# Optimization experiments

Hardware: AMD Instinct MI355X
Metric: run time of the kernel (lower is better)

Reference implementation:

```python
import jax, jax.numpy as jnp
import numpy as np

D_MODEL = 768
NUM_HEADS = 12
D_HEAD = D_MODEL // NUM_HEADS
LN_EPS = 1e-5


def layer_norm(x, w, b):
    m = jnp.mean(x, axis=-1, keepdims=True)
    v = jnp.mean(jnp.square(x - m), axis=-1, keepdims=True)
    return (x - m) * jax.lax.rsqrt(v + LN_EPS) * w + b


def setup_inputs() -> dict:
    key = jax.random.key(0)
    ks = jax.random.split(key, 10)
    B, P, NQ, D = 16, 197, 8, D_MODEL
    s = 1.0 / np.sqrt(D)
    return {
        "q_x": jax.random.normal(ks[0], (1, NQ, D), jnp.float32),
        "kv_x": jax.random.normal(ks[1], (B, P, D), jnp.float32),
        "pair_pos_embedding": jax.random.normal(ks[2], (2 * P, D), jnp.float32) * 0.02,
        "q_w": jax.random.normal(ks[3], (D, D), jnp.float32) * s,
        "q_b": jnp.zeros((D,), jnp.float32),
        "kv_w": jax.random.normal(ks[4], (D, D), jnp.float32) * s,
        "kv_b": jnp.zeros((D,), jnp.float32),
        "out_w": jax.random.normal(ks[5], (D, D), jnp.float32) * s,
        "out_b": jnp.zeros((D,), jnp.float32),
        "lnq_w": jnp.ones((D,), jnp.float32),
        "lnq_b": jnp.zeros((D,), jnp.float32),
        "lnkv_w": jnp.ones((D,), jnp.float32),
        "lnkv_b": jnp.zeros((D,), jnp.float32),
    }


def reference(q_x, kv_x, pair_pos_embedding, q_w, q_b, kv_w, kv_b,
              out_w, out_b, lnq_w, lnq_b, lnkv_w, lnkv_b):
    H, dh = NUM_HEADS, D_HEAD
    scale = dh ** -0.5
    _, NQ, D = q_x.shape
    B, P, _ = kv_x.shape

    # q path: Linear -> LN -> split heads -> [1, H, NQ, dh]
    q = layer_norm(q_x @ q_w.T + q_b, lnq_w, lnq_b)
    q = q.reshape(1, NQ, H, dh).transpose(0, 2, 1, 3)  # [1,H,NQ,dh]

    # kv path: Linear -> LN -> split heads -> [B, H, P, dh]
    kv = layer_norm(kv_x @ kv_w.T + kv_b, lnkv_w, lnkv_b)
    kv = kv.reshape(B, P, H, dh).transpose(0, 2, 1, 3)  # [B,H,P,dh]

    # pairwise expansion: kv_concat[i*B+j] = cat(kv[i], kv[j]) along token dim
    kv_rep = jnp.repeat(kv, B, axis=0)          # [B^2,H,P,dh] (repeat_interleave)
    kv_til = jnp.tile(kv, (B, 1, 1, 1))         # [B^2,H,P,dh]
    kv_cat = jnp.concatenate([kv_rep, kv_til], axis=2)  # [B^2,H,2P,dh]

    # positional bias: [2P, D] -> [1, H, 2P, dh]
    pos = pair_pos_embedding.reshape(1, 2 * P, H, dh).transpose(0, 2, 1, 3)
    kv_cat = kv_cat + pos

    scores = jnp.einsum('bhqd,bhpd->bhqp', jnp.broadcast_to(q, (B * B, H, NQ, dh)), kv_cat) * scale
    attn = jax.nn.softmax(scores, axis=-1)      # [B^2,H,NQ,2P]

    v1 = jnp.einsum('bhqp,bhpd->bhqd', attn[..., :P], kv_cat[:, :, :P, :])
    v2 = jnp.einsum('bhqp,bhpd->bhqd', attn[..., P:], kv_cat[:, :, P:, :])
    values = (v1 - v2).transpose(0, 2, 1, 3).reshape(B * B, NQ, D)
    return values @ out_w.T + out_b
```

## Files before the change

kernel.cpp:

```cpp
#include <hip/hip_runtime.h>
#include <hip/hip_bf16.h>
#include <math.h>

#define D_MODEL 768
#define NHEADS  12
#define DHEAD   64
#define NQR     8
#define BB      16
#define PP      197
#define NPAIR   256
#define MKV     (BB*PP)
#define LN_EPSF 1e-5f
#define SCALEF  0.125f

#define KTOT  2304
#define KSPLIT 3
#define KPER  (KTOT/KSPLIT)
#define MPAD  3200
#define BM 128
#define BN 128
#define BK 64

typedef __attribute__((ext_vector_type(8))) short short8v;
typedef __attribute__((ext_vector_type(4))) float float4v;

__device__ __forceinline__ void gload16(const void* g, void* l){
  __builtin_amdgcn_global_load_lds(
      (const __attribute__((address_space(1))) unsigned int*)g,
      (__attribute__((address_space(3))) unsigned int*)l, 16, 0, 0);
}

__global__ __launch_bounds__(256) void qgemm_kernel(
    const float* __restrict__ qx, const float* __restrict__ qw,
    float* __restrict__ qy)
{
  __shared__ float xs[NQR*D_MODEL];
  int tid = threadIdx.x;
  for (int e = tid*4; e < NQR*D_MODEL; e += 1024)
    *(float4*)&xs[e] = *(const float4*)&qx[e];
  __syncthreads();
  int col = tid >> 5, lane = tid & 31;
  int c = blockIdx.x*8 + col;
  const float* wr = qw + (size_t)c*D_MODEL;
  float acc[NQR] = {};
  for (int k = lane*4; k < D_MODEL; k += 128){
    float4 w4 = *(const float4*)&wr[k];
    #pragma unroll
    for (int q = 0; q < NQR; q++){
      float4 x4 = *(const float4*)&xs[q*D_MODEL + k];
      acc[q] += x4.x*w4.x + x4.y*w4.y + x4.z*w4.z + x4.w*w4.w;
    }
  }
  #pragma unroll
  for (int q = 0; q < NQR; q++){
    float a = acc[q];
    for (int off = 16; off >= 1; off >>= 1) a += __shfl_xor(a, off, 32);
    if (lane == 0) qy[q*D_MODEL + c] = a;
  }
}

__global__ __launch_bounds__(192) void pack_both_kernel(
    const float* __restrict__ kvx, const float* __restrict__ kvw,
    __hip_bfloat16* __restrict__ Ab, __hip_bfloat16* __restrict__ Wb)
{
  int b = blockIdx.x, t = threadIdx.x;
  const float* X; __hip_bfloat16* Y; int valid, mode, m;
  if (b < MPAD){ X = kvx; Y = Ab; valid = MKV;     mode = 0; m = b; }
  else         { X = kvw; Y = Wb; valid = D_MODEL; mode = 1; m = b - MPAD; }
  int k = t*4;
  float4 v = (m < valid) ? *(const float4*)&X[(size_t)m*D_MODEL + k]
                         : make_float4(0.f,0.f,0.f,0.f);
  float xsv[4] = {v.x, v.y, v.z, v.w};
  unsigned short hu[4], lu[4];
  #pragma unroll
  for (int i = 0; i < 4; i++){
    __hip_bfloat16 h = __float2bfloat16(xsv[i]);
    float hf = __bfloat162float(h);
    __hip_bfloat16 l = __float2bfloat16(xsv[i] - hf);
    hu[i] = *(unsigned short*)&h;
    lu[i] = *(unsigned short*)&l;
  }
  ushort4 hv = {hu[0], hu[1], hu[2], hu[3]};
  ushort4 lv = {lu[0], lu[1], lu[2], lu[3]};
  ushort4* row = (ushort4*)(Y + (size_t)m*KTOT);
  int s = k >> 2;
  if (mode == 0){ row[s] = hv; row[s+192] = hv; row[s+384] = lv; }
  else          { row[s] = hv; row[s+192] = lv; row[s+384] = hv; }
}

__global__ __launch_bounds__(256) void gemm_mfma_kernel(
    const __hip_bfloat16* __restrict__ Ab, const __hip_bfloat16* __restrict__ Wb,
    float* __restrict__ Cp)
{
  __shared__ __hip_bfloat16 As[BM*BK];
  __shared__ __hip_bfloat16 Bs[BN*BK];
  int tid = threadIdx.x;
  int wave = tid >> 6, lane = tid & 63;
  int m0 = blockIdx.x*BM, n0 = blockIdx.y*BN, kt = blockIdx.z;
  int wr = wave >> 1, wc = wave & 1;

  float4v acc[4][4];
  #pragma unroll
  for (int i = 0; i < 4; i++)
    #pragma unroll
    for (int j = 0; j < 4; j++)
      acc[i][j] = (float4v){0.f, 0.f, 0.f, 0.f};

  int sbase = wave*256;
  for (int st = 0; st < KPER/BK; ++st){
    int k0 = kt*KPER + st*BK;
    __syncthreads();
    #pragma unroll
    for (int i = 0; i < 4; i++){
      int s  = sbase + i*64 + lane;
      int r  = s >> 3, kg = s & 7;
      int kgg = kg ^ (r & 7);
      gload16(Ab + (size_t)(m0 + r)*KTOT + k0 + kgg*8, (char*)As + (size_t)s*16);
      gload16(Wb + (size_t)(n0 + r)*KTOT + k0 + kgg*8, (char*)Bs + (size_t)s*16);
    }
    __syncthreads();
    #pragma unroll
    for (int ks = 0; ks < 2; ks++){
      int kq = ks*4 + (lane >> 4);
      short8v af[4], bf[4];
      #pragma unroll
      for (int t = 0; t < 4; t++){
        int ar = wr*64 + t*16 + (lane & 15);
        int as_ = ar*8 + (kq ^ (ar & 7));
        af[t] = *(const short8v*)((const char*)As + (size_t)as_*16);
        int br = wc*64 + t*16 + (lane & 15);
        int bs_ = br*8 + (kq ^ (br & 7));
        bf[t] = *(const short8v*)((const char*)Bs + (size_t)bs_*16);
      }
      #pragma unroll
      for (int i = 0; i < 4; i++)
        #pragma unroll
        for (int j = 0; j < 4; j++)
          acc[i][j] = __builtin_amdgcn_mfma_f32_16x16x32_bf16(af[i], bf[j], acc[i][j], 0, 0, 0);
    }
  }

  float* C = Cp + (size_t)kt*MKV*D_MODEL;
  #pragma unroll
  for (int i = 0; i < 4; i++){
    int mb = m0 + wr*64 + i*16 + ((lane >> 4) << 2);
    #pragma unroll
    for (int j = 0; j < 4; j++){
      int n = n0 + wc*64 + j*16 + (lane & 15);
      #pragma unroll
      for (int r = 0; r < 4; r++){
        int m = mb + r;
        if (m < MKV) C[(size_t)m*D_MODEL + n] = acc[i][j][r];
      }
    }
  }
}

__global__ __launch_bounds__(256) void ln_rows_kernel(
    const float* __restrict__ Y, const float* __restrict__ bias,
    const float* __restrict__ lnw, const float* __restrict__ lnb,
    float* __restrict__ out)
{
  __shared__ float red[256], red2[256];
  int r = blockIdx.x, tid = threadIdx.x;
  const float* yr = Y + (size_t)r*D_MODEL;
  float x0 = yr[tid      ] + bias[tid      ];
  float x1 = yr[tid + 256] + bias[tid + 256];
  float x2 = yr[tid + 512] + bias[tid + 512];
  red[tid] = x0 + x1 + x2; red2[tid] = x0*x0 + x1*x1 + x2*x2;
  __syncthreads();
  for (int st = 128; st > 0; st >>= 1){
    if (tid < st){ red[tid] += red[tid+st]; red2[tid] += red2[tid+st]; }
    __syncthreads();
  }
  float mean = red[0]*(1.f/768.f);
  float var  = red2[0]*(1.f/768.f) - mean*mean;
  float inv  = rsqrtf(var + LN_EPSF);
  float* orow = out + (size_t)r*D_MODEL;
  orow[tid      ] = (x0-mean)*inv*lnw[tid      ] + lnb[tid      ];
  orow[tid + 256] = (x1-mean)*inv*lnw[tid + 256] + lnb[tid + 256];
  orow[tid + 512] = (x2-mean)*inv*lnw[tid + 512] + lnb[tid + 512];
}

__global__ __launch_bounds__(256) void ln_rows3_kernel(
    const float* __restrict__ Y0, const float* __restrict__ Y1,
    const float* __restrict__ Y2, const float* __restrict__ bias,
    const float* __restrict__ lnw, const float* __restrict__ lnb,
    float* __restrict__ out)
{
  __shared__ float red[256], red2[256];
  int r = blockIdx.x, tid = threadIdx.x;
  const float* y0 = Y0 + (size_t)r*D_MODEL;
  const float* y1 = Y1 + (size_t)r*D_MODEL;
  const float* y2 = Y2 + (size_t)r*D_MODEL;
  float x0 = y0[tid      ] + y1[tid      ] + y2[tid      ] + bias[tid      ];
  float x1 = y0[tid + 256] + y1[tid + 256] + y2[tid + 256] + bias[tid + 256];
  float x2 = y0[tid + 512] + y1[tid + 512] + y2[tid + 512] + bias[tid + 512];
  red[tid] = x0 + x1 + x2; red2[tid] = x0*x0 + x1*x1 + x2*x2;
  __syncthreads();
  for (int st = 128; st > 0; st >>= 1){
    if (tid < st){ red[tid] += red[tid+st]; red2[tid] += red2[tid+st]; }
    __syncthreads();
  }
  float mean = red[0]*(1.f/768.f);
  float var  = red2[0]*(1.f/768.f) - mean*mean;
  float inv  = rsqrtf(var + LN_EPSF);
  float* orow = out + (size_t)r*D_MODEL;
  orow[tid      ] = (x0-mean)*inv*lnw[tid      ] + lnb[tid      ];
  orow[tid + 256] = (x1-mean)*inv*lnw[tid + 256] + lnb[tid + 256];
  orow[tid + 512] = (x2-mean)*inv*lnw[tid + 512] + lnb[tid + 512];
}

__global__ __launch_bounds__(256) void rank_partials_kernel(
    const float* __restrict__ kv_ln, const float* __restrict__ q_ln,
    const float* __restrict__ ppe,
    float* __restrict__ m1O, float* __restrict__ z1O, float* __restrict__ u1O,
    float* __restrict__ m2O, float* __restrict__ z2O, float* __restrict__ u2O)
{
  __shared__ float A[PP*65];
  __shared__ float qs[NQR*64];
  __shared__ float E[NQR*PP];
  int r = blockIdx.x, h = blockIdx.y, half = blockIdx.z;
  int tid = threadIdx.x;

  for (int e = tid; e < NQR*64; e += 256){
    int q = e >> 6, d = e & 63;
    qs[e] = q_ln[q*D_MODEL + h*64 + d];
  }
  for (int e = tid; e < PP*64; e += 256){
    int p = e >> 6, d = e & 63;
    A[p*65 + d] = kv_ln[((size_t)(r*PP + p))*D_MODEL + h*64 + d]
                + ppe[((size_t)(half*PP + p))*D_MODEL + h*64 + d];
  }
  __syncthreads();

  int q = tid >> 5, sub = tid & 31;
  float s[7];
  #pragma unroll
  for (int i = 0; i < 7; i++) s[i] = 0.f;
  for (int d = 0; d < 64; d++){
    float qv = qs[q*64 + d];
    #pragma unroll
    for (int i = 0; i < 7; i++){
      int p = sub + 32*i;
      int pc = p < PP ? p : PP-1;
      s[i] += qv * A[pc*65 + d];
    }
  }
  float mloc = -1e30f;
  #pragma unroll
  for (int i = 0; i < 7; i++){
    int p = sub + 32*i;
    s[i] = (p < PP) ? s[i]*SCALEF : -1e30f;
    mloc = fmaxf(mloc, s[i]);
  }
  for (int off = 16; off >= 1; off >>= 1)
    mloc = fmaxf(mloc, __shfl_xor(mloc, off, 32));
  float zloc = 0.f;
  #pragma unroll
  for (int i = 0; i < 7; i++){
    int p = sub + 32*i;
    float e = __expf(s[i] - mloc);
    if (p < PP){ E[q*PP + p] = e; zloc += e; }
  }
  for (int off = 16; off >= 1; off >>= 1)
    zloc += __shfl_xor(zloc, off, 32);

  int idx = (r*NHEADS + h)*NQR + q;
  float* mO = half ? m2O : m1O;
  float* zO = half ? z2O : z1O;
  float* uO = half ? u2O : u1O;
  if (sub == 0){ mO[idx] = mloc; zO[idx] = zloc; }
  __syncthreads();

  float u0 = 0.f, u1 = 0.f;
  for (int p = 0; p < PP; p++){
    float e = E[q*PP + p];
    u0 += e * A[p*65 + sub];
    u1 += e * A[p*65 + sub + 32];
  }
  uO[(size_t)idx*64 + sub]      = u0;
  uO[(size_t)idx*64 + sub + 32] = u1;
}

__global__ __launch_bounds__(256) void proj_kernel(
    const float* __restrict__ u1, const float* __restrict__ u2,
    const float* __restrict__ ow, float* __restrict__ p1, float* __restrict__ p2)
{
  __shared__ float Us[128][65];
  __shared__ float Ws[128][65];
  int h = blockIdx.x, n0 = blockIdx.y*128;
  const float* U = blockIdx.z ? u2 : u1;
  float*       P = blockIdx.z ? p2 : p1;
  int tid = threadIdx.x;
  for (int e = tid; e < 128*16; e += 256){
    int m = e >> 4, d4 = (e & 15) << 2;
    int i = m >> 3, q = m & 7;
    float4 v = *(const float4*)&U[(((size_t)i*NHEADS + h)*NQR + q)*64 + d4];
    Us[m][d4] = v.x; Us[m][d4+1] = v.y; Us[m][d4+2] = v.z; Us[m][d4+3] = v.w;
  }
  for (int e = tid; e < 128*16; e += 256){
    int n = e >> 4, d4 = (e & 15) << 2;
    float4 v = *(const float4*)&ow[((size_t)(n0+n))*D_MODEL + h*64 + d4];
    Ws[n][d4] = v.x; Ws[n][d4+1] = v.y; Ws[n][d4+2] = v.z; Ws[n][d4+3] = v.w;
  }
  __syncthreads();
  int tx = tid & 15, ty = tid >> 4;
  float acc[8][8] = {};
  for (int k = 0; k < 64; k++){
    float ur[8], wr[8];
    #pragma unroll
    for (int r = 0; r < 8; r++) ur[r] = Us[ty*8 + r][k];
    #pragma unroll
    for (int c = 0; c < 8; c++) wr[c] = Ws[tx*8 + c][k];
    #pragma unroll
    for (int r = 0; r < 8; r++)
      #pragma unroll
      for (int c = 0; c < 8; c++)
        acc[r][c] += ur[r]*wr[c];
  }
  #pragma unroll
  for (int r = 0; r < 8; r++){
    int m = ty*8 + r, i = m >> 3, q = m & 7;
    float* prow = P + (((size_t)i*NHEADS + h)*NQR + q)*D_MODEL + n0 + tx*8;
    *(float4*)&prow[0] = make_float4(acc[r][0], acc[r][1], acc[r][2], acc[r][3]);
    *(float4*)&prow[4] = make_float4(acc[r][4], acc[r][5], acc[r][6], acc[r][7]);
  }
}

__global__ __launch_bounds__(256) void combine_out_kernel(
    const float* __restrict__ m1, const float* __restrict__ z1,
    const float* __restrict__ m2, const float* __restrict__ z2,
    const float* __restrict__ p1, const float* __restrict__ p2,
    const float* __restrict__ out_b, float* __restrict__ out)
{
  __shared__ float c1s[NHEADS], c2s[NHEADS];
  int pair = blockIdx.x, q = blockIdx.y, tid = threadIdx.x;
  int i = pair >> 4, j = pair & 15;
  if (tid < NHEADS){
    int h = tid;
    int ii = (i*NHEADS + h)*NQR + q;
    int jj = (j*NHEADS + h)*NQR + q;
    float mi = m1[ii], mj = m2[jj];
    float mm = fmaxf(mi, mj);
    float a1 = __expf(mi - mm), a2 = __expf(mj - mm);
    float rden = 1.f / (a1*z1[ii] + a2*z2[jj]);
    c1s[h] = a1*rden; c2s[h] = a2*rden;
  }
  __syncthreads();
  float* orow = out + ((size_t)(pair*NQR + q))*D_MODEL;
  for (int nn = tid; nn < D_MODEL; nn += 256){
    float acc = out_b[nn];
    #pragma unroll
    for (int h = 0; h < NHEADS; h++){
      acc += c1s[h]*p1[(((size_t)i*NHEADS + h)*NQR + q)*D_MODEL + nn]
           - c2s[h]*p2[(((size_t)j*NHEADS + h)*NQR + q)*D_MODEL + nn];
    }
    orow[nn] = acc;
  }
}

extern "C" void kernel_launch(void* const* d_in, const int* in_sizes, int n_in,
                              void* d_out, int out_size, void* d_ws, size_t ws_size,
                              hipStream_t stream)
{
  const float* q_x    = (const float*)d_in[0];
  const float* kv_x   = (const float*)d_in[1];
  const float* ppe    = (const float*)d_in[2];
  const float* q_w    = (const float*)d_in[3];
  const float* q_b    = (const float*)d_in[4];
  const float* kv_w   = (const float*)d_in[5];
  const float* kv_b   = (const float*)d_in[6];
  const float* out_w  = (const float*)d_in[7];
  const float* out_b  = (const float*)d_in[8];
  const float* lnq_w  = (const float*)d_in[9];
  const float* lnq_b  = (const float*)d_in[10];
  const float* lnkv_w = (const float*)d_in[11];
  const float* lnkv_b = (const float*)d_in[12];
  float* out = (float*)d_out;

  float* ws    = (float*)d_ws;
  float* q_y   = ws;
  float* q_ln  = q_y  + NQR*D_MODEL;
  float* Abuf_f = q_ln + NQR*D_MODEL;
  float* Wbuf_f = Abuf_f + (size_t)MPAD*KTOT/2;
  float* C0    = Wbuf_f + (size_t)D_MODEL*KTOT/2;
  float* C1    = C0 + (size_t)MKV*D_MODEL;
  float* C2    = C1 + (size_t)MKV*D_MODEL;

  __hip_bfloat16* Abuf = (__hip_bfloat16*)Abuf_f;
  __hip_bfloat16* Wbuf = (__hip_bfloat16*)Wbuf_f;

  float* kv_ln = Abuf_f;
  float* m1    = Wbuf_f;
  float* z1    = m1 + BB*NHEADS*NQR;
  float* m2    = z1 + BB*NHEADS*NQR;
  float* z2    = m2 + BB*NHEADS*NQR;
  float* u1    = z2 + BB*NHEADS*NQR;
  float* u2    = u1 + BB*NHEADS*NQR*DHEAD;
  float* p1    = C0;
  float* p2    = p1 + (size_t)BB*NHEADS*NQR*D_MODEL;

  qgemm_kernel<<<96, 256, 0, stream>>>(q_x, q_w, q_y);
  ln_rows_kernel<<<NQR, 256, 0, stream>>>(q_y, q_b, lnq_w, lnq_b, q_ln);

  pack_both_kernel<<<MPAD + D_MODEL, 192, 0, stream>>>(kv_x, kv_w, Abuf, Wbuf);

  gemm_mfma_kernel<<<dim3(MPAD/BM, D_MODEL/BN, KSPLIT), 256, 0, stream>>>(
      Abuf, Wbuf, C0);

  ln_rows3_kernel<<<MKV, 256, 0, stream>>>(C0, C1, C2, kv_b, lnkv_w, lnkv_b, kv_ln);

  rank_partials_kernel<<<dim3(BB, NHEADS, 2), 256, 0, stream>>>(
      kv_ln, q_ln, ppe, m1, z1, u1, m2, z2, u2);

  proj_kernel<<<dim3(NHEADS, D_MODEL/128, 2), 256, 0, stream>>>(
      u1, u2, out_w, p1, p2);

  combine_out_kernel<<<dim3(NPAIR, NQR), 256, 0, stream>>>(
      m1, z1, m2, z2, p1, p2, out_b, out);
}
```

Measured before the change: 182.4 us.

## Fuse q projection+LN into pack kernel and merge rank partials with out-projection

```diff
diff --git a/kernel.cpp b/kernel.cpp
--- a/kernel.cpp
+++ b/kernel.cpp
@@ -30,62 +30,77 @@
       (__attribute__((address_space(3))) unsigned int*)l, 16, 0, 0);
 }
 
-__global__ __launch_bounds__(256) void qgemm_kernel(
+__global__ __launch_bounds__(192) void pack_q_kernel(
+    const float* __restrict__ kvx, const float* __restrict__ kvw,
+    __hip_bfloat16* __restrict__ Ab, __hip_bfloat16* __restrict__ Wb,
     const float* __restrict__ qx, const float* __restrict__ qw,
-    float* __restrict__ qy)
-{
-  __shared__ float xs[NQR*D_MODEL];
-  int tid = threadIdx.x;
-  for (int e = tid*4; e < NQR*D_MODEL; e += 1024)
-    *(float4*)&xs[e] = *(const float4*)&qx[e];
-  __syncthreads();
-  int col = tid >> 5, lane = tid & 31;
-  int c = blockIdx.x*8 + col;
-  const float* wr = qw + (size_t)c*D_MODEL;
-  float acc[NQR] = {};
-  for (int k = lane*4; k < D_MODEL; k += 128){
-    float4 w4 = *(const float4*)&wr[k];
-    #pragma unroll
-    for (int q = 0; q < NQR; q++){
-      float4 x4 = *(const float4*)&xs[q*D_MODEL + k];
-      acc[q] += x4.x*w4.x + x4.y*w4.y + x4.z*w4.z + x4.w*w4.w;
-    }
-  }
-  #pragma unroll
-  for (int q = 0; q < NQR; q++){
-    float a = acc[q];
-    for (int off = 16; off >= 1; off >>= 1) a += __shfl_xor(a, off, 32);
-    if (lane == 0) qy[q*D_MODEL + c] = a;
-  }
-}
-
-__global__ __launch_bounds__(192) void pack_both_kernel(
-    const float* __restrict__ kvx, const float* __restrict__ kvw,
-    __hip_bfloat16* __restrict__ Ab, __hip_bfloat16* __restrict__ Wb)
+    const float* __restrict__ qb, const float* __restrict__ lnqw,
+    const float* __restrict__ lnqb, float* __restrict__ qln)
 {
   int b = blockIdx.x, t = threadIdx.x;
-  const float* X; __hip_bfloat16* Y; int valid, mode, m;
-  if (b < MPAD){ X = kvx; Y = Ab; valid = MKV;     mode = 0; m = b; }
-  else         { X = kvw; Y = Wb; valid = D_MODEL; mode = 1; m = b - MPAD; }
-  int k = t*4;
-  float4 v = (m < valid) ? *(const float4*)&X[(size_t)m*D_MODEL + k]
-                         : make_float4(0.f,0.f,0.f,0.f);
-  float xsv[4] = {v.x, v.y, v.z, v.w};
-  unsigned short hu[4], lu[4];
-  #pragma unroll
-  for (int i = 0; i < 4; i++){
-    __hip_bfloat16 h = __float2bfloat16(xsv[i]);
-    float hf = __bfloat162float(h);
-    __hip_bfloat16 l = __float2bfloat16(xsv[i] - hf);
-    hu[i] = *(unsigned short*)&h;
-    lu[i] = *(unsigned short*)&l;
-  }
-  ushort4 hv = {hu[0], hu[1], hu[2], hu[3]};
-  ushort4 lv = {lu[0], lu[1], lu[2], lu[3]};
-  ushort4* row = (ushort4*)(Y + (size_t)m*KTOT);
-  int s = k >> 2;
-  if (mode == 0){ row[s] = hv; row[s+192] = hv; row[s+384] = lv; }
-  else          { row[s] = hv; row[s+192] = lv; row[s+384] = hv; }
+  if (b < MPAD + D_MODEL){
+    const float* X; __hip_bfloat16* Y; int valid, mode, m;
+    if (b < MPAD){ X = kvx; Y = Ab; valid = MKV;     mode = 0; m = b; }
+    else         { X = kvw; Y = Wb; valid = D_MODEL; mode = 1; m = b - MPAD; }
+    int k = t*4;
+    float4 v = (m < valid) ? *(const float4*)&X[(size_t)m*D_MODEL + k]
+                           : make_float4(0.f,0.f,0.f,0.f);
+    float xsv[4] = {v.x, v.y, v.z, v.w};
+    unsigned short hu[4], lu[4];
+    #pragma unroll
+    for (int i = 0; i < 4; i++){
+      __hip_bfloat16 h = __float2bfloat16(xsv[i]);
+      float hf = __bfloat162float(h);
+      __hip_bfloat16 l = __float2bfloat16(xsv[i] - hf);
+      hu[i] = *(unsigned short*)&h;
+      lu[i] = *(unsigned short*)&l;
+    }
+    ushort4 hv = {hu[0], hu[1], hu[2], hu[3]};
+    ushort4 lv = {lu[0], lu[1], lu[2], lu[3]};
+    ushort4* row = (ushort4*)(Y + (size_t)m*KTOT);
+    int s = k >> 2;
+    if (mode == 0){ row[s] = hv; row[s+192] = hv; row[s+384] = lv; }
+    else          { row[s] = hv; row[s+192] = lv; row[s+384] = hv; }
+    return;
+  }
+  __shared__ float xrow[D_MODEL];
+  __shared__ float yrow[D_MODEL];
+  __shared__ float ws1[3], ws2[3];
+  int r = b - (MPAD + D_MODEL);
+  *(float4*)&xrow[t*4] = *(const float4*)&qx[r*D_MODEL + t*4];
+  __syncthreads();
+  float yv[4];
+  #pragma unroll
+  for (int c4 = 0; c4 < 4; c4++){
+    int c = t + 192*c4;
+    const float* wr = qw + (size_t)c*D_MODEL;
+    float a = 0.f;
+    for (int k = 0; k < D_MODEL; k += 4){
+      float4 w4 = *(const float4*)&wr[k];
+      a += xrow[k]*w4.x + xrow[k+1]*w4.y + xrow[k+2]*w4.z + xrow[k+3]*w4.w;
+    }
+    yv[c4] = a + qb[c];
+    yrow[c] = yv[c4];
+  }
+  float s1 = yv[0]+yv[1]+yv[2]+yv[3];
+  float s2 = yv[0]*yv[0]+yv[1]*yv[1]+yv[2]*yv[2]+yv[3]*yv[3];
+  for (int off = 32; off >= 1; off >>= 1){
+    s1 += __shfl_xor(s1, off);
+    s2 += __shfl_xor(s2, off);
+  }
+  int wave = t >> 6, lane = t & 63;
+  if (lane == 0){ ws1[wave] = s1; ws2[wave] = s2; }
+  __syncthreads();
+  float S1 = ws1[0]+ws1[1]+ws1[2];
+  float S2 = ws2[0]+ws2[1]+ws2[2];
+  float mean = S1*(1.f/768.f);
+  float var  = S2*(1.f/768.f) - mean*mean;
+  float inv  = rsqrtf(var + LN_EPSF);
+  #pragma unroll
+  for (int c4 = 0; c4 < 4; c4++){
+    int c = t + 192*c4;
+    qln[r*D_MODEL + c] = (yrow[c]-mean)*inv*lnqw[c] + lnqb[c];
+  }
 }
 
 __global__ __launch_bounds__(256) void gemm_mfma_kernel(
@@ -156,32 +171,6 @@
   }
 }
 
-__global__ __launch_bounds__(256) void ln_rows_kernel(
-    const float* __restrict__ Y, const float* __restrict__ bias,
-    const float* __restrict__ lnw, const float* __restrict__ lnb,
-    float* __restrict__ out)
-{
-  __shared__ float red[256], red2[256];
-  int r = blockIdx.x, tid = threadIdx.x;
-  const float* yr = Y + (size_t)r*D_MODEL;
-  float x0 = yr[tid      ] + bias[tid      ];
-  float x1 = yr[tid + 256] + bias[tid + 256];
-  float x2 = yr[tid + 512] + bias[tid + 512];
-  red[tid] = x0 + x1 + x2; red2[tid] = x0*x0 + x1*x1 + x2*x2;
-  __syncthreads();
-  for (int st = 128; st > 0; st >>= 1){
-    if (tid < st){ red[tid] += red[tid+st]; red2[tid] += red2[tid+st]; }
-    __syncthreads();
-  }
-  float mean = red[0]*(1.f/768.f);
-  float var  = red2[0]*(1.f/768.f) - mean*mean;
-  float inv  = rsqrtf(var + LN_EPSF);
-  float* orow = out + (size_t)r*D_MODEL;
-  orow[tid      ] = (x0-mean)*inv*lnw[tid      ] + lnb[tid      ];
-  orow[tid + 256] = (x1-mean)*inv*lnw[tid + 256] + lnb[tid + 256];
-  orow[tid + 512] = (x2-mean)*inv*lnw[tid + 512] + lnb[tid + 512];
-}
-
 __global__ __launch_bounds__(256) void ln_rows3_kernel(
     const float* __restrict__ Y0, const float* __restrict__ Y1,
     const float* __restrict__ Y2, const float* __restrict__ bias,
@@ -211,120 +200,108 @@
   orow[tid + 512] = (x2-mean)*inv*lnw[tid + 512] + lnb[tid + 512];
 }
 
-__global__ __launch_bounds__(256) void rank_partials_kernel(
+__global__ __launch_bounds__(256) void rank_proj_kernel(
     const float* __restrict__ kv_ln, const float* __restrict__ q_ln,
-    const float* __restrict__ ppe,
-    float* __restrict__ m1O, float* __restrict__ z1O, float* __restrict__ u1O,
-    float* __restrict__ m2O, float* __restrict__ z2O, float* __restrict__ u2O)
+    const float* __restrict__ ppe, const float* __restrict__ ow,
+    float* __restrict__ m1O, float* __restrict__ z1O,
+    float* __restrict__ m2O, float* __restrict__ z2O,
+    float* __restrict__ p1, float* __restrict__ p2)
 {
   __shared__ float A[PP*65];
   __shared__ float qs[NQR*64];
   __shared__ float E[NQR*PP];
-  int r = blockIdx.x, h = blockIdx.y, half = blockIdx.z;
+  __shared__ float Us[16*64];
+  int r = blockIdx.x, h = blockIdx.y;
   int tid = threadIdx.x;
 
   for (int e = tid; e < NQR*64; e += 256){
     int q = e >> 6, d = e & 63;
     qs[e] = q_ln[q*D_MODEL + h*64 + d];
   }
-  for (int e = tid; e < PP*64; e += 256){
-    int p = e >> 6, d = e & 63;
-    A[p*65 + d] = kv_ln[((size_t)(r*PP + p))*D_MODEL + h*64 + d]
-                + ppe[((size_t)(half*PP + p))*D_MODEL + h*64 + d];
-  }
-  __syncthreads();
-
-  int q = tid >> 5, sub = tid & 31;
-  float s[7];
-  #pragma unroll
-  for (int i = 0; i < 7; i++) s[i] = 0.f;
-  for (int d = 0; d < 64; d++){
-    float qv = qs[q*64 + d];
+
+  for (int half = 0; half < 2; half++){
+    __syncthreads();
+    for (int e = tid; e < PP*64; e += 256){
+      int p = e >> 6, d = e & 63;
+      A[p*65 + d] = kv_ln[((size_t)(r*PP + p))*D_MODEL + h*64 + d]
+                  + ppe[((size_t)(half*PP + p))*D_MODEL + h*64 + d];
+    }
+    __syncthreads();
+
+    int q = tid >> 5, sub = tid & 31;
+    float s[7];
+    #pragma unroll
+    for (int i = 0; i < 7; i++) s[i] = 0.f;
+    for (int d = 0; d < 64; d++){
+      float qv = qs[q*64 + d];
+      #pragma unroll
+      for (int i = 0; i < 7; i++){
+        int p = sub + 32*i;
+        int pc = p < PP ? p : PP-1;
+        s[i] += qv * A[pc*65 + d];
+      }
+    }
+    float mloc = -1e30f;
     #pragma unroll
     for (int i = 0; i < 7; i++){
       int p = sub + 32*i;
-      int pc = p < PP ? p : PP-1;
-      s[i] += qv * A[pc*65 + d];
-    }
-  }
-  float mloc = -1e30f;
-  #pragma unroll
-  for (int i = 0; i < 7; i++){
-    int p = sub + 32*i;
-    s[i] = (p < PP) ? s[i]*SCALEF : -1e30f;
-    mloc = fmaxf(mloc, s[i]);
-  }
-  for (int off = 16; off >= 1; off >>= 1)
-    mloc = fmaxf(mloc, __shfl_xor(mloc, off, 32));
-  float zloc = 0.f;
-  #pragma unroll
-  for (int i = 0; i < 7; i++){
-    int p = sub + 32*i;
-    float e = __expf(s[i] - mloc);
-    if (p < PP){ E[q*PP + p] = e; zloc += e; }
-  }
-  for (int off = 16; off >= 1; off >>= 1)
-    zloc += __shfl_xor(zloc, off, 32);
-
-  int idx = (r*NHEADS + h)*NQR + q;
-  float* mO = half ? m2O : m1O;
-  float* zO = half ? z2O : z1O;
-  float* uO = half ? u2O : u1O;
-  if (sub == 0){ mO[idx] = mloc; zO[idx] = zloc; }
-  __syncthreads();
-
-  float u0 = 0.f, u1 = 0.f;
-  for (int p = 0; p < PP; p++){
-    float e = E[q*PP + p];
-    u0 += e * A[p*65 + sub];
-    u1 += e * A[p*65 + sub + 32];
-  }
-  uO[(size_t)idx*64 + sub]      = u0;
-  uO[(size_t)idx*64 + sub + 32] = u1;
-}
-
-__global__ __launch_bounds__(256) void proj_kernel(
-    const float* __restrict__ u1, const float* __restrict__ u2,
-    const float* __restrict__ ow, float* __restrict__ p1, float* __restrict__ p2)
-{
-  __shared__ float Us[128][65];
-  __shared__ float Ws[128][65];
-  int h = blockIdx.x, n0 = blockIdx.y*128;
-  const float* U = blockIdx.z ? u2 : u1;
-  float*       P = blockIdx.z ? p2 : p1;
-  int tid = threadIdx.x;
-  for (int e = tid; e < 128*16; e += 256){
-    int m = e >> 4, d4 = (e & 15) << 2;
-    int i = m >> 3, q = m & 7;
-    float4 v = *(const float4*)&U[(((size_t)i*NHEADS + h)*NQR + q)*64 + d4];
-    Us[m][d4] = v.x; Us[m][d4+1] = v.y; Us[m][d4+2] = v.z; Us[m][d4+3] = v.w;
-  }
-  for (int e = tid; e < 128*16; e += 256){
-    int n = e >> 4, d4 = (e & 15) << 2;
-    float4 v = *(const float4*)&ow[((size_t)(n0+n))*D_MODEL + h*64 + d4];
-    Ws[n][d4] = v.x; Ws[n][d4+1] = v.y; Ws[n][d4+2] = v.z; Ws[n][d4+3] = v.w;
-  }
-  __syncthreads();
-  int tx = tid & 15, ty = tid >> 4;
-  float acc[8][8] = {};
-  for (int k = 0; k < 64; k++){
-    float ur[8], wr[8];
-    #pragma unroll
-    for (int r = 0; r < 8; r++) ur[r] = Us[ty*8 + r][k];
-    #pragma unroll
-    for (int c = 0; c < 8; c++) wr[c] = Ws[tx*8 + c][k];
-    #pragma unroll
-    for (int r = 0; r < 8; r++)
-      #pragma unroll
-      for (int c = 0; c < 8; c++)
-        acc[r][c] += ur[r]*wr[c];
-  }
-  #pragma unroll
-  for (int r = 0; r < 8; r++){
-    int m = ty*8 + r, i = m >> 3, q = m & 7;
-    float* prow = P + (((size_t)i*NHEADS + h)*NQR + q)*D_MODEL + n0 + tx*8;
-    *(float4*)&prow[0] = make_float4(acc[r][0], acc[r][1], acc[r][2], acc[r][3]);
-    *(float4*)&prow[4] = make_float4(acc[r][4], acc[r][5], acc[r][6], acc[r][7]);
+      s[i] = (p < PP) ? s[i]*SCALEF : -1e30f;
+      mloc = fmaxf(mloc, s[i]);
+    }
+    for (int off = 16; off >= 1; off >>= 1)
+      mloc = fmaxf(mloc, __shfl_xor(mloc, off, 32));
+    float zloc = 0.f;
+    #pragma unroll
+    for (int i = 0; i < 7; i++){
+      int p = sub + 32*i;
+      float e = __expf(s[i] - mloc);
+      if (p < PP){ E[q*PP + p] = e; zloc += e; }
+    }
+    for (int off = 16; off >= 1; off >>= 1)
+      zloc += __shfl_xor(zloc, off, 32);
+
+    int idx = (r*NHEADS + h)*NQR + q;
+    if (sub == 0){
+      if (half){ m2O[idx] = mloc; z2O[idx] = zloc; }
+      else     { m1O[idx] = mloc; z1O[idx] = zloc; }
+    }
+    __syncthreads();
+
+    float u0 = 0.f, u1 = 0.f;
+    for (int p = 0; p < PP; p++){
+      float e = E[q*PP + p];
+      u0 += e * A[p*65 + sub];
+      u1 += e * A[p*65 + sub + 32];
+    }
+    Us[(half*NQR + q)*64 + sub]      = u0;
+    Us[(half*NQR + q)*64 + sub + 32] = u1;
+  }
+  __syncthreads();
+
+  float acc[16][3];
+  #pragma unroll
+  for (int m = 0; m < 16; m++){ acc[m][0]=0.f; acc[m][1]=0.f; acc[m][2]=0.f; }
+  const float* owh = ow + h*64;
+  for (int d4 = 0; d4 < 64; d4 += 4){
+    float4 w0 = *(const float4*)&owh[(size_t)(tid      )*D_MODEL + d4];
+    float4 w1 = *(const float4*)&owh[(size_t)(tid + 256)*D_MODEL + d4];
+    float4 w2 = *(const float4*)&owh[(size_t)(tid + 512)*D_MODEL + d4];
+    #pragma unroll
+    for (int m = 0; m < 16; m++){
+      float4 u = *(const float4*)&Us[m*64 + d4];
+      acc[m][0] += u.x*w0.x + u.y*w0.y + u.z*w0.z + u.w*w0.w;
+      acc[m][1] += u.x*w1.x + u.y*w1.y + u.z*w1.z + u.w*w1.w;
+      acc[m][2] += u.x*w2.x + u.y*w2.y + u.z*w2.z + u.w*w2.w;
+    }
+  }
+  #pragma unroll
+  for (int q = 0; q < NQR; q++){
+    size_t base = (((size_t)r*NHEADS + h)*NQR + q)*D_MODEL;
+    #pragma unroll
+    for (int j = 0; j < 3; j++){
+      p1[base + tid + 256*j] = acc[q][j];
+      p2[base + tid + 256*j] = acc[8 + q][j];
+    }
   }
 }
 
@@ -380,8 +357,7 @@
   float* out = (float*)d_out;
 
   float* ws    = (float*)d_ws;
-  float* q_y   = ws;
-  float* q_ln  = q_y  + NQR*D_MODEL;
+  float* q_ln  = ws;
   float* Abuf_f = q_ln + NQR*D_MODEL;
   float* Wbuf_f = Abuf_f + (size_t)MPAD*KTOT/2;
   float* C0    = Wbuf_f + (size_t)D_MODEL*KTOT/2;
@@ -396,26 +372,19 @@
   float* z1    = m1 + BB*NHEADS*NQR;
   float* m2    = z1 + BB*NHEADS*NQR;
   float* z2    = m2 + BB*NHEADS*NQR;
-  float* u1    = z2 + BB*NHEADS*NQR;
-  float* u2    = u1 + BB*NHEADS*NQR*DHEAD;
   float* p1    = C0;
   float* p2    = p1 + (size_t)BB*NHEADS*NQR*D_MODEL;
 
-  qgemm_kernel<<<96, 256, 0, stream>>>(q_x, q_w, q_y);
-  ln_rows_kernel<<<NQR, 256, 0, stream>>>(q_y, q_b, lnq_w, lnq_b, q_ln);
-
-  pack_both_kernel<<<MPAD + D_MODEL, 192, 0, stream>>>(kv_x, kv_w, Abuf, Wbuf);
+  pack_q_kernel<<<MPAD + D_MODEL + NQR, 192, 0, stream>>>(
+      kv_x, kv_w, Abuf, Wbuf, q_x, q_w, q_b, lnq_w, lnq_b, q_ln);
 
   gemm_mfma_kernel<<<dim3(MPAD/BM, D_MODEL/BN, KSPLIT), 256, 0, stream>>>(
       Abuf, Wbuf, C0);
 
   ln_rows3_kernel<<<MKV, 256, 0, stream>>>(C0, C1, C2, kv_b, lnkv_w, lnkv_b, kv_ln);
 
-  rank_partials_kernel<<<dim3(BB, NHEADS, 2), 256, 0, stream>>>(
-      kv_ln, q_ln, ppe, m1, z1, u1, m2, z2, u2);
-
-  proj_kernel<<<dim3(NHEADS, D_MODEL/128, 2), 256, 0, stream>>>(
-      u1, u2, out_w, p1, p2);
+  rank_proj_kernel<<<dim3(BB, NHEADS), 256, 0, stream>>>(
+      kv_ln, q_ln, ppe, out_w, m1, z1, m2, z2, p1, p2);
 
   combine_out_kernel<<<dim3(NPAIR, NQR), 256, 0, stream>>>(
       m1, z1, m2, z2, p1, p2, out_b, out);
```

Result: slower. 242.2 us (+32.8%).
